# Performance work log

Hardware: AMD Instinct MI355X
Metric: run time of the kernel (lower is better)

## Reference

```python
import jax, jax.numpy as jnp
import numpy as np

SCALE = 1.0

def setup_inputs() -> dict:
    key = jax.random.key(0)
    k1, k2 = jax.random.split(key)
    features = jax.random.normal(k1, (16, 512, 128, 128), dtype=jnp.float32)
    probs = jax.random.normal(k2, (16, 19, 128, 128), dtype=jnp.float32)
    return {"features": features, "probs": probs}

def reference(features, probs):
    B, K, H, W = probs.shape
    C = features.shape[1]
    p = probs.reshape(B, K, H * W)               # [B, K, HW]
    f = features.reshape(B, C, H * W)            # [B, C, HW]
    attn = jax.nn.softmax(SCALE * p, axis=2)     # softmax over spatial dim
    # ocr_context[b, k, c] = sum_hw attn[b,k,hw] * f[b,c,hw]
    ctx = jnp.einsum('bks,bcs->bkc', attn, f)    # [B, K, C]
    return jnp.transpose(ctx, (0, 2, 1))[..., None]  # [B, C, K, 1]
```

## Files before the change

### kernel.cpp

```cpp
#include <hip/hip_runtime.h>
#include <math.h>

#define BATCH 16
#define KCLS  19
#define CCH   512
#define HW    16384

#define KSPLIT 16
#define KB     (HW / KSPLIT)
#define BK     64
#define NCHUNK (KB / BK)
#define NT     128
#define KPAD   20
#define BCN    (BATCH * CCH)

typedef __attribute__((ext_vector_type(8))) short  short8;
typedef __attribute__((ext_vector_type(4))) float  floatx4;

typedef __attribute__((address_space(3))) void*        lds_ptr_t;
typedef const __attribute__((address_space(1))) void*  gbl_ptr_t;

static __device__ __forceinline__ ushort f2bf(float x) {
  unsigned u = __float_as_uint(x);
  return (ushort)((u + 0x7FFFu + ((u >> 16) & 1u)) >> 16);
}

static __device__ __forceinline__ short8 pack8(float4 a, float4 b) {
  short8 v;
  v[0] = (short)f2bf(a.x); v[1] = (short)f2bf(a.y);
  v[2] = (short)f2bf(a.z); v[3] = (short)f2bf(a.w);
  v[4] = (short)f2bf(b.x); v[5] = (short)f2bf(b.y);
  v[6] = (short)f2bf(b.z); v[7] = (short)f2bf(b.w);
  return v;
}

__global__ __launch_bounds__(256) void softmax_stats_kernel(
    const float* __restrict__ probs, float* __restrict__ stats) {
  const int bk = blockIdx.x;
  const float4* row = (const float4*)(probs + (size_t)bk * HW);
  const int tid  = threadIdx.x;
  const int lane = tid & 63;
  const int wave = tid >> 6;
  __shared__ float red[4];

  float m = -1e30f;
  for (int i = tid; i < HW / 4; i += 256) {
    float4 v = row[i];
    m = fmaxf(m, fmaxf(fmaxf(v.x, v.y), fmaxf(v.z, v.w)));
  }
  for (int off = 32; off > 0; off >>= 1) m = fmaxf(m, __shfl_xor(m, off));
  if (lane == 0) red[wave] = m;
  __syncthreads();
  m = fmaxf(fmaxf(red[0], red[1]), fmaxf(red[2], red[3]));

  float s = 0.f;
  for (int i = tid; i < HW / 4; i += 256) {
    float4 v = row[i];
    s += __expf(v.x - m) + __expf(v.y - m) + __expf(v.z - m) + __expf(v.w - m);
  }
  for (int off = 32; off > 0; off >>= 1) s += __shfl_xor(s, off);
  __syncthreads();
  if (lane == 0) red[wave] = s;
  __syncthreads();
  if (tid == 0) {
    float total = red[0] + red[1] + red[2] + red[3];
    stats[2 * bk]     = m;
    stats[2 * bk + 1] = 1.0f / total;
  }
}

__global__ __launch_bounds__(256, 1) void gather_mfma(
    const float* __restrict__ feat, const float* __restrict__ probs,
    const float* __restrict__ stats, float* __restrict__ part) {
  __shared__ __align__(16) float Fs[2][NT][BK];
  __shared__ __align__(16) short As[2][32][BK];

  const int bid = blockIdx.x;
  const int b   = bid & 15;
  const int r1  = bid >> 4;
  const int ct  = r1 & 3;
  const int ks  = r1 >> 2;
  const int k0  = ks * KB;

  const int tid  = threadIdx.x;
  const int wave = tid >> 6;
  const int lane = tid & 63;

  const float* fbase = feat  + ((size_t)(b * CCH + ct * NT)) * HW + k0;
  const float* pbase = probs + ((size_t)b * KCLS) * HW + k0;

  const int  prow = tid >> 3, pg = tid & 7;
  const bool pact = (tid < KCLS * 8);
  float pm = 0.f, pinv = 0.f;
  if (pact) {
    pm   = stats[2 * (b * KCLS + prow)];
    pinv = stats[2 * (b * KCLS + prow) + 1];
  }

  floatx4 acc00 = {0,0,0,0}, acc01 = {0,0,0,0}, acc10 = {0,0,0,0}, acc11 = {0,0,0,0};
  float4 pA, pB;

#define DMA_CHUNK(buf, c)                                                       \
  {                                                                             \
    char* lb = ((char*)Fs) + (buf) * 32768 + wave * 8192;                       \
    _Pragma("unroll")                                                           \
    for (int i = 0; i < 8; i++) {                                               \
      int ch = wave * 32 + i * 4 + (lane >> 4);                                 \
      const float* src = fbase + (size_t)ch * HW + (c) * BK                     \
                         + (((lane & 15) ^ (ch & 7)) << 2);                     \
      __builtin_amdgcn_global_load_lds((gbl_ptr_t)src,                          \
                                       (lds_ptr_t)(lb + i * 1024), 16, 0, 0);   \
    }                                                                           \
  }

#define PLOAD(c)                                                                \
  if (pact) {                                                                   \
    const float* q = pbase + (size_t)prow * HW + (c) * BK + pg * 8;             \
    pA = *(const float4*)q;  pB = *(const float4*)(q + 4);                      \
  }

#define PSTAGE(buf)                                                             \
  if (pact) {                                                                   \
    short8 v;                                                                   \
    v[0] = (short)f2bf(__expf(pA.x - pm) * pinv);                               \
    v[1] = (short)f2bf(__expf(pA.y - pm) * pinv);                               \
    v[2] = (short)f2bf(__expf(pA.z - pm) * pinv);                               \
    v[3] = (short)f2bf(__expf(pA.w - pm) * pinv);                               \
    v[4] = (short)f2bf(__expf(pB.x - pm) * pinv);                               \
    v[5] = (short)f2bf(__expf(pB.y - pm) * pinv);                               \
    v[6] = (short)f2bf(__expf(pB.z - pm) * pinv);                               \
    v[7] = (short)f2bf(__expf(pB.w - pm) * pinv);                               \
    *(short8*)((char*)As + (buf) * 4096 + prow * 128 + ((pg ^ (prow & 7)) << 4)) = v; \
  }

#define GEMMC(buf)                                                              \
  {                                                                             \
    const char* Ab = (const char*)As + (buf) * 4096;                            \
    const char* Fb = (const char*)Fs + (buf) * 32768;                           \
    _Pragma("unroll")                                                           \
    for (int kt = 0; kt < 2; kt++) {                                            \
      const int gA  = kt * 4 + (lane >> 4);                                     \
      const int rm0 = lane & 15;                                                \
      const int rm1 = 16 + rm0;                                                 \
      const int ch0 = wave * 32 + (lane & 15);                                  \
      const int ch1 = ch0 + 16;                                                 \
      short8 a0 = *(const short8*)(Ab + rm0 * 128 + ((gA ^ (rm0 & 7)) << 4));   \
      short8 a1 = *(const short8*)(Ab + rm1 * 128 + ((gA ^ (rm1 & 7)) << 4));   \
      float4 b0lo = *(const float4*)(Fb + ch0 * 256 + (((2 * gA)     ^ (ch0 & 7)) << 4)); \
      float4 b0hi = *(const float4*)(Fb + ch0 * 256 + (((2 * gA + 1) ^ (ch0 & 7)) << 4)); \
      float4 b1lo = *(const float4*)(Fb + ch1 * 256 + (((2 * gA)     ^ (ch1 & 7)) << 4)); \
      float4 b1hi = *(const float4*)(Fb + ch1 * 256 + (((2 * gA + 1) ^ (ch1 & 7)) << 4)); \
      short8 b0 = pack8(b0lo, b0hi);                                            \
      short8 b1 = pack8(b1lo, b1hi);                                            \
      acc00 = __builtin_amdgcn_mfma_f32_16x16x32_bf16(a0, b0, acc00, 0, 0, 0);  \
      acc01 = __builtin_amdgcn_mfma_f32_16x16x32_bf16(a0, b1, acc01, 0, 0, 0);  \
      acc10 = __builtin_amdgcn_mfma_f32_16x16x32_bf16(a1, b0, acc10, 0, 0, 0);  \
      acc11 = __builtin_amdgcn_mfma_f32_16x16x32_bf16(a1, b1, acc11, 0, 0, 0);  \
    }                                                                           \
  }

  DMA_CHUNK(0, 0);
  PLOAD(0);
  PSTAGE(0);
  __syncthreads();

  for (int c = 0; c < NCHUNK; c++) {
    const int cur = c & 1, nxt = cur ^ 1;
    if (c + 1 < NCHUNK) { DMA_CHUNK(nxt, c + 1); PLOAD(c + 1); }
    GEMMC(cur);
    if (c + 1 < NCHUNK) PSTAGE(nxt);
    __syncthreads();
  }

  {
    const int chb = ct * NT + wave * 32;
    const int cl  = lane & 15;
    const int rb  = (lane >> 4) * 4;
    size_t bc0 = (size_t)b * CCH + chb + cl;
    size_t bc1 = bc0 + 16;
    float* p0 = part + ((size_t)ks * BCN + bc0) * KPAD + rb;
    float* p1 = part + ((size_t)ks * BCN + bc1) * KPAD + rb;
    *(float4*)p0 = *(float4*)&acc00;
    *(float4*)p1 = *(float4*)&acc01;
    if (rb == 0) {
      *(float4*)(p0 + 16) = *(float4*)&acc10;
      *(float4*)(p1 + 16) = *(float4*)&acc11;
    }
  }
#undef DMA_CHUNK
#undef PLOAD
#undef PSTAGE
#undef GEMMC
}

__global__ __launch_bounds__(256) void reduce_kernel(
    const float* __restrict__ part, float* __restrict__ out) {
  const int gid = blockIdx.x * 256 + threadIdx.x;
  const int bc = gid / KPAD, r = gid - bc * KPAD;
  if (r < KCLS) {
    float s = 0.f;
    #pragma unroll
    for (int k = 0; k < KSPLIT; k++)
      s += part[(size_t)k * (BCN * KPAD) + gid];
    out[(size_t)bc * KCLS + r] = s;
  }
}

extern "C" void kernel_launch(void* const* d_in, const int* in_sizes, int n_in,
                              void* d_out, int out_size, void* d_ws, size_t ws_size,
                              hipStream_t stream) {
  const float* feat  = (const float*)d_in[0];
  const float* probs = (const float*)d_in[1];
  float* out   = (float*)d_out;
  float* stats = (float*)d_ws;
  float* part  = (float*)((char*)d_ws + 4096);

  softmax_stats_kernel<<<BATCH * KCLS, 256, 0, stream>>>(probs, stats);
  gather_mfma<<<BATCH * 4 * KSPLIT, 256, 0, stream>>>(feat, probs, stats, part);
  reduce_kernel<<<(BCN * KPAD) / 256, 256, 0, stream>>>(part, out);
}
```

Baseline: 139.3 us.

## Load features directly into registers and precompute full softmax slice in LDS

Stops staging feature tiles through LDS with async global-to-LDS DMA. Each lane now loads its MFMA B-operand features straight from global memory into registers, double-buffered across chunks. The softmax-weighted probability slice for the whole K-split (19 rows by 1024 columns in bf16) is computed once up front into LDS, so the main loop needs no barriers. The risks are register pressure from the two register sets, less coalesced global loads, and the loss of latency hiding from the async DMA.

```diff
diff --git a/kernel.cpp b/kernel.cpp
--- a/kernel.cpp
+++ b/kernel.cpp
@@ -15,10 +15,8 @@
 #define BCN    (BATCH * CCH)
 
 typedef __attribute__((ext_vector_type(8))) short  short8;
+typedef __attribute__((ext_vector_type(4))) short  short4v;
 typedef __attribute__((ext_vector_type(4))) float  floatx4;
-
-typedef __attribute__((address_space(3))) void*        lds_ptr_t;
-typedef const __attribute__((address_space(1))) void*  gbl_ptr_t;
 
 static __device__ __forceinline__ ushort f2bf(float x) {
   unsigned u = __float_as_uint(x);
@@ -69,11 +67,12 @@
   }
 }
 
+struct FSet { float4 v[8]; };
+
 __global__ __launch_bounds__(256, 1) void gather_mfma(
     const float* __restrict__ feat, const float* __restrict__ probs,
     const float* __restrict__ stats, float* __restrict__ part) {
-  __shared__ __align__(16) float Fs[2][NT][BK];
-  __shared__ __align__(16) short As[2][32][BK];
+  __shared__ __align__(16) short A_all[KCLS][KB];
 
   const int bid = blockIdx.x;
   const int b   = bid & 15;
@@ -89,69 +88,40 @@
   const float* fbase = feat  + ((size_t)(b * CCH + ct * NT)) * HW + k0;
   const float* pbase = probs + ((size_t)b * KCLS) * HW + k0;
 
-  const int  prow = tid >> 3, pg = tid & 7;
-  const bool pact = (tid < KCLS * 8);
-  float pm = 0.f, pinv = 0.f;
-  if (pact) {
-    pm   = stats[2 * (b * KCLS + prow)];
-    pinv = stats[2 * (b * KCLS + prow) + 1];
+  const int ch0 = wave * 32 + (lane & 15);
+  const int ch1 = ch0 + 16;
+  const float* fptr0 = fbase + (size_t)ch0 * HW + (lane >> 4) * 8;
+  const float* fptr1 = fbase + (size_t)ch1 * HW + (lane >> 4) * 8;
+
+  floatx4 acc00 = {0,0,0,0}, acc01 = {0,0,0,0}, acc10 = {0,0,0,0}, acc11 = {0,0,0,0};
+
+  FSet sA, sB;
+
+#define LOADF(S, c)                                                             \
+  {                                                                             \
+    const int cb = (c) * BK;                                                    \
+    S.v[0] = *(const float4*)(fptr0 + cb);                                      \
+    S.v[1] = *(const float4*)(fptr0 + cb + 4);                                  \
+    S.v[2] = *(const float4*)(fptr1 + cb);                                      \
+    S.v[3] = *(const float4*)(fptr1 + cb + 4);                                  \
+    S.v[4] = *(const float4*)(fptr0 + cb + 32);                                 \
+    S.v[5] = *(const float4*)(fptr0 + cb + 36);                                 \
+    S.v[6] = *(const float4*)(fptr1 + cb + 32);                                 \
+    S.v[7] = *(const float4*)(fptr1 + cb + 36);                                 \
   }
 
-  floatx4 acc00 = {0,0,0,0}, acc01 = {0,0,0,0}, acc10 = {0,0,0,0}, acc11 = {0,0,0,0};
-  float4 pA, pB;
-
-#define DMA_CHUNK(buf, c)                                                       \
+#define GEMMC(S, c)                                                             \
   {                                                                             \
-    char* lb = ((char*)Fs) + (buf) * 32768 + wave * 8192;                       \
-    _Pragma("unroll")                                                           \
-    for (int i = 0; i < 8; i++) {                                               \
-      int ch = wave * 32 + i * 4 + (lane >> 4);                                 \
-      const float* src = fbase + (size_t)ch * HW + (c) * BK                     \
-                         + (((lane & 15) ^ (ch & 7)) << 2);                     \
-      __builtin_amdgcn_global_load_lds((gbl_ptr_t)src,                          \
-                                       (lds_ptr_t)(lb + i * 1024), 16, 0, 0);   \
-    }                                                                           \
-  }
-
-#define PLOAD(c)                                                                \
-  if (pact) {                                                                   \
-    const float* q = pbase + (size_t)prow * HW + (c) * BK + pg * 8;             \
-    pA = *(const float4*)q;  pB = *(const float4*)(q + 4);                      \
-  }
-
-#define PSTAGE(buf)                                                             \
-  if (pact) {                                                                   \
-    short8 v;                                                                   \
-    v[0] = (short)f2bf(__expf(pA.x - pm) * pinv);                               \
-    v[1] = (short)f2bf(__expf(pA.y - pm) * pinv);                               \
-    v[2] = (short)f2bf(__expf(pA.z - pm) * pinv);                               \
-    v[3] = (short)f2bf(__expf(pA.w - pm) * pinv);                               \
-    v[4] = (short)f2bf(__expf(pB.x - pm) * pinv);                               \
-    v[5] = (short)f2bf(__expf(pB.y - pm) * pinv);                               \
-    v[6] = (short)f2bf(__expf(pB.z - pm) * pinv);                               \
-    v[7] = (short)f2bf(__expf(pB.w - pm) * pinv);                               \
-    *(short8*)((char*)As + (buf) * 4096 + prow * 128 + ((pg ^ (prow & 7)) << 4)) = v; \
-  }
-
-#define GEMMC(buf)                                                              \
-  {                                                                             \
-    const char* Ab = (const char*)As + (buf) * 4096;                            \
-    const char* Fb = (const char*)Fs + (buf) * 32768;                           \
+    const char* Ab = (const char*)A_all;                                        \
+    const int rm0  = lane & 15;                                                 \
+    const int rm1  = 16 + (rm0 < 3 ? rm0 : 2);    \
     _Pragma("unroll")                                                           \
     for (int kt = 0; kt < 2; kt++) {                                            \
-      const int gA  = kt * 4 + (lane >> 4);                                     \
-      const int rm0 = lane & 15;                                                \
-      const int rm1 = 16 + rm0;                                                 \
-      const int ch0 = wave * 32 + (lane & 15);                                  \
-      const int ch1 = ch0 + 16;                                                 \
-      short8 a0 = *(const short8*)(Ab + rm0 * 128 + ((gA ^ (rm0 & 7)) << 4));   \
-      short8 a1 = *(const short8*)(Ab + rm1 * 128 + ((gA ^ (rm1 & 7)) << 4));   \
-      float4 b0lo = *(const float4*)(Fb + ch0 * 256 + (((2 * gA)     ^ (ch0 & 7)) << 4)); \
-      float4 b0hi = *(const float4*)(Fb + ch0 * 256 + (((2 * gA + 1) ^ (ch0 & 7)) << 4)); \
-      float4 b1lo = *(const float4*)(Fb + ch1 * 256 + (((2 * gA)     ^ (ch1 & 7)) << 4)); \
-      float4 b1hi = *(const float4*)(Fb + ch1 * 256 + (((2 * gA + 1) ^ (ch1 & 7)) << 4)); \
-      short8 b0 = pack8(b0lo, b0hi);                                            \
-      short8 b1 = pack8(b1lo, b1hi);                                            \
+      const int g = (c) * 8 + kt * 4 + (lane >> 4);                             \
+      short8 a0 = *(const short8*)(Ab + rm0 * 2048 + ((g ^ (rm0 & 7)) << 4));   \
+      short8 a1 = *(const short8*)(Ab + rm1 * 2048 + ((g ^ (rm1 & 7)) << 4));   \
+      short8 b0 = pack8(S.v[kt * 4 + 0], S.v[kt * 4 + 1]);                      \
+      short8 b1 = pack8(S.v[kt * 4 + 2], S.v[kt * 4 + 3]);                      \
       acc00 = __builtin_amdgcn_mfma_f32_16x16x32_bf16(a0, b0, acc00, 0, 0, 0);  \
       acc01 = __builtin_amdgcn_mfma_f32_16x16x32_bf16(a0, b1, acc01, 0, 0, 0);  \
       acc10 = __builtin_amdgcn_mfma_f32_16x16x32_bf16(a1, b0, acc10, 0, 0, 0);  \
@@ -159,17 +129,26 @@
     }                                                                           \
   }
 
-  DMA_CHUNK(0, 0);
-  PLOAD(0);
-  PSTAGE(0);
+  LOADF(sA, 0);
+
+  for (int j = 0; j < KCLS; j++) {
+    float m  = stats[2 * (b * KCLS + j)];
+    float iv = stats[2 * (b * KCLS + j) + 1];
+    float4 p = *(const float4*)(pbase + (size_t)j * HW + tid * 4);
+    short4v v;
+    v[0] = (short)f2bf(__expf(p.x - m) * iv);
+    v[1] = (short)f2bf(__expf(p.y - m) * iv);
+    v[2] = (short)f2bf(__expf(p.z - m) * iv);
+    v[3] = (short)f2bf(__expf(p.w - m) * iv);
+    *(short4v*)((char*)A_all + j * 2048 + (((tid >> 1) ^ (j & 7)) << 4) + (tid & 1) * 8) = v;
+  }
   __syncthreads();
 
-  for (int c = 0; c < NCHUNK; c++) {
-    const int cur = c & 1, nxt = cur ^ 1;
-    if (c + 1 < NCHUNK) { DMA_CHUNK(nxt, c + 1); PLOAD(c + 1); }
-    GEMMC(cur);
-    if (c + 1 < NCHUNK) PSTAGE(nxt);
-    __syncthreads();
+  for (int c = 0; c < NCHUNK; c += 2) {
+    LOADF(sB, c + 1);
+    GEMMC(sA, c);
+    if (c + 2 < NCHUNK) LOADF(sA, c + 2);
+    GEMMC(sB, c + 1);
   }
 
   {
@@ -187,9 +166,7 @@
       *(float4*)(p1 + 16) = *(float4*)&acc11;
     }
   }
-#undef DMA_CHUNK
-#undef PLOAD
-#undef PSTAGE
+#undef LOADF
 #undef GEMMC
 }
 
```

Measured after the change: 137.1 us. About the same (-1.6%).
